# Kernel tuning notes

Hardware: AMD Instinct MI355X
Metric: run time of the kernel (lower is better)

The kernel has to match this reference:

```python
import jax, jax.numpy as jnp
import numpy as np
import math

B, S = 512, 50
L, U = 40000, 20000
D_MODEL, D_LOC, D_USR, D_T, H, D_FF = 80, 56, 12, 12, 4, 160
DH = D_MODEL // H


def _layernorm(x, g, b, eps=1e-5):
    m = x.mean(-1, keepdims=True)
    v = ((x - m) ** 2).mean(-1, keepdims=True)
    return (x - m) / jnp.sqrt(v + eps) * g + b


def setup_inputs() -> dict:
    key = jax.random.key(0)
    ks = jax.random.split(key, 16)
    loc_seq = jax.random.randint(ks[0], (B, S), 0, L)
    user_seq = jax.random.randint(ks[1], (B, S), 0, U)
    weekday_seq = jax.random.randint(ks[2], (B, S), 0, 7)
    start_min_seq = jax.random.uniform(ks[3], (B, S), jnp.float32, 0.0, 1440.0)
    dur_seq = jax.random.uniform(ks[4], (B, S), jnp.float32, 0.0, 600.0)
    diff_seq = jax.random.randint(ks[5], (B, S), 0, 7)
    mask = jnp.ones((B, S), dtype=bool)
    # sinusoidal positional-encoding buffer (60, 80), as in __init__
    pos = np.arange(60, dtype=np.float32)[:, None]
    div = np.exp(np.arange(0, D_MODEL, 2, dtype=np.float32) * (-math.log(10000.0) / D_MODEL))
    pe = np.zeros((60, D_MODEL), dtype=np.float32)
    pe[:, 0::2] = np.sin(pos * div)
    pe[:, 1::2] = np.cos(pos * div)
    g = lambda k, shape: jax.random.normal(k, shape, jnp.float32) * 0.02
    return dict(
        loc_seq=loc_seq, user_seq=user_seq, weekday_seq=weekday_seq,
        start_min_seq=start_min_seq, dur_seq=dur_seq, diff_seq=diff_seq, mask=mask,
        loc_emb=jax.random.normal(ks[6], (L, D_LOC), jnp.float32) * 0.01,
        user_emb=jax.random.normal(ks[7], (U, D_USR), jnp.float32) * 0.01,
        tproj_w=g(ks[8], (6, D_T)), tproj_b=jnp.zeros((D_T,), jnp.float32),
        in_norm_g=jnp.ones((D_MODEL,), jnp.float32), in_norm_b=jnp.zeros((D_MODEL,), jnp.float32),
        attn_in_w=g(ks[9], (3 * D_MODEL, D_MODEL)), attn_in_b=jnp.zeros((3 * D_MODEL,), jnp.float32),
        attn_out_w=g(ks[10], (D_MODEL, D_MODEL)), attn_out_b=jnp.zeros((D_MODEL,), jnp.float32),
        norm1_g=jnp.ones((D_MODEL,), jnp.float32), norm1_b=jnp.zeros((D_MODEL,), jnp.float32),
        ff_w1=g(ks[11], (D_MODEL, D_FF)), ff_b1=jnp.zeros((D_FF,), jnp.float32),
        ff_w2=g(ks[12], (D_FF, D_MODEL)), ff_b2=jnp.zeros((D_MODEL,), jnp.float32),
        norm2_g=jnp.ones((D_MODEL,), jnp.float32), norm2_b=jnp.zeros((D_MODEL,), jnp.float32),
        pred_w1=g(ks[13], (D_MODEL, D_FF)), pred_b1=jnp.zeros((D_FF,), jnp.float32),
        pred_w2=g(ks[14], (D_FF, L)), pred_b2=jnp.zeros((L,), jnp.float32),
        recency_decay=jnp.float32(0.62), freq_weight=jnp.float32(2.2),
        history_scale=jnp.float32(11.0), model_weight=jnp.float32(0.22),
        pe=jnp.asarray(pe),
    )


def _history_scores(loc_seq, mask, recency_decay, freq_weight, history_scale):
    # Vectorized scatter-max (recency) + scatter-add (frequency) over the whole
    # (B, S) index set -- replaces the per-timestep python loop of the original.
    maskf = mask.astype(jnp.float32)
    time_from_end = jnp.arange(S - 1, -1, -1, dtype=jnp.float32)  # seq_len - t - 1
    rw = jnp.power(recency_decay, time_from_end)[None, :] * maskf  # (B, S)
    bidx = jnp.broadcast_to(jnp.arange(B)[:, None], (B, S))
    rec = jnp.zeros((B, L), jnp.float32).at[bidx, loc_seq].max(rw)
    freq = jnp.zeros((B, L), jnp.float32).at[bidx, loc_seq].add(maskf)
    freq = freq / jnp.clip(freq.max(axis=1, keepdims=True), 1.0)
    return history_scale * (rec + freq_weight * freq)


def _forward(loc_seq, user_seq, weekday_seq, start_min_seq, dur_seq, diff_seq, mask,
             loc_emb, user_emb, tproj_w, tproj_b, in_norm_g, in_norm_b,
             attn_in_w, attn_in_b, attn_out_w, attn_out_b, norm1_g, norm1_b,
             ff_w1, ff_b1, ff_w2, ff_b2, norm2_g, norm2_b,
             pred_w1, pred_b1, pred_w2, pred_b2,
             recency_decay, freq_weight, history_scale, model_weight, pe):
    hist = _history_scores(loc_seq, mask, recency_decay, freq_weight, history_scale)
    le = loc_emb[loc_seq]                       # (B, S, 56)
    ue = user_emb[user_seq]                     # (B, S, 12)
    tr = (start_min_seq / 60.0) / 24.0 * 2.0 * jnp.pi
    wr = weekday_seq.astype(jnp.float32) / 7.0 * 2.0 * jnp.pi
    tf = jnp.stack([jnp.sin(tr), jnp.cos(tr), jnp.log1p(dur_seq) / 8.0,
                    jnp.sin(wr), jnp.cos(wr), diff_seq.astype(jnp.float32) / 7.0], axis=-1)
    te = tf @ tproj_w + tproj_b                 # (B, S, 12)
    x = jnp.concatenate([le, ue, te], axis=-1)  # (B, S, 80)
    x = _layernorm(x, in_norm_g, in_norm_b)
    x = x + pe[:S][None]
    # multi-head self-attention with key padding mask (dropout=eval mode)
    qkv = x @ attn_in_w.T + attn_in_b
    q, k, v = jnp.split(qkv, 3, axis=-1)
    q = q.reshape(B, S, H, DH)
    k = k.reshape(B, S, H, DH)
    v = v.reshape(B, S, H, DH)
    scores = jnp.einsum('bqhd,bkhd->bhqk', q, k) / jnp.sqrt(jnp.float32(DH))
    scores = jnp.where(mask[:, None, None, :], scores, -jnp.inf)
    attn = jax.nn.softmax(scores, axis=-1)
    ao = jnp.einsum('bhqk,bkhd->bqhd', attn, v).reshape(B, S, D_MODEL)
    ao = ao @ attn_out_w.T + attn_out_b
    x = _layernorm(x + ao, norm1_g, norm1_b)
    ff = jax.nn.gelu(x @ ff_w1 + ff_b1, approximate=False) @ ff_w2 + ff_b2
    x = _layernorm(x + ff, norm2_g, norm2_b)
    seq_lens = mask.sum(axis=1) - 1             # index of last valid token
    last = jnp.take_along_axis(x, seq_lens[:, None, None], axis=1)[:, 0]  # (B, 80)
    logits = jax.nn.gelu(last @ pred_w1 + pred_b1, approximate=False) @ pred_w2 + pred_b2
    return hist + model_weight * (jax.nn.softmax(logits, axis=1) * L)


def reference(loc_seq, user_seq, weekday_seq, start_min_seq, dur_seq, diff_seq, mask,
              loc_emb, user_emb, tproj_w, tproj_b, in_norm_g, in_norm_b,
              attn_in_w, attn_in_b, attn_out_w, attn_out_b, norm1_g, norm1_b,
              ff_w1, ff_b1, ff_w2, ff_b2, norm2_g, norm2_b,
              pred_w1, pred_b1, pred_w2, pred_b2,
              recency_decay, freq_weight, history_scale, model_weight, pe):
    return _forward(loc_seq, user_seq, weekday_seq, start_min_seq, dur_seq, diff_seq, mask,
                    loc_emb, user_emb, tproj_w, tproj_b, in_norm_g, in_norm_b,
                    attn_in_w, attn_in_b, attn_out_w, attn_out_b, norm1_g, norm1_b,
                    ff_w1, ff_b1, ff_w2, ff_b2, norm2_g, norm2_b,
                    pred_w1, pred_b1, pred_w2, pred_b2,
                    recency_decay, freq_weight, history_scale, model_weight, pe)
```

## Files before the change

### kernel.cpp

```cpp
#include <hip/hip_runtime.h>
#include <math.h>

#define BB 512
#define SS 50
#define LL 40000
#define DM 80
#define DLOC 56
#define DUSR 12
#define HH 4
#define DH 20
#define DFF 160
#define XP 81
#define NPREP 157

typedef __attribute__((ext_vector_type(8))) short short8v;
typedef __attribute__((ext_vector_type(4))) float f32x4;

__device__ __forceinline__ unsigned short f2bf(float f) {
    unsigned u = __float_as_uint(f);
    u += 0x7fffu + ((u >> 16) & 1u);
    return (unsigned short)(u >> 16);
}

__device__ __forceinline__ float gelu_exact(float x) {
    return 0.5f * x * (1.0f + erff(x * 0.70710678118654752f));
}

__global__ __launch_bounds__(256) void k_front(
        const int* __restrict__ loc_seq, const int* __restrict__ user_seq,
        const int* __restrict__ wd_seq, const float* __restrict__ start_seq,
        const float* __restrict__ dur_seq, const int* __restrict__ diff_seq,
        const float* __restrict__ loc_emb, const float* __restrict__ user_emb,
        const float* __restrict__ tproj_w, const float* __restrict__ tproj_b,
        const float* __restrict__ in_g, const float* __restrict__ in_b,
        const float* __restrict__ pe,
        const float* __restrict__ Wqkv, const float* __restrict__ bqkv,
        const float* __restrict__ aw, const float* __restrict__ ab,
        const float* __restrict__ n1g, const float* __restrict__ n1b,
        const float* __restrict__ w1, const float* __restrict__ b1,
        const float* __restrict__ w2, const float* __restrict__ b2,
        const float* __restrict__ n2g, const float* __restrict__ n2b,
        const float* __restrict__ pw1, const float* __restrict__ pb1,
        const float* __restrict__ pw2,
        const float* __restrict__ p_decay, const float* __restrict__ p_fw,
        const float* __restrict__ p_hs,
        float* __restrict__ histval, int* __restrict__ histloc,
        unsigned short* __restrict__ gvec, unsigned short* __restrict__ Bp,
        float* __restrict__ rowsum) {
    int tid = threadIdx.x;

    if (blockIdx.x >= BB) {
        int n = (blockIdx.x - BB) * 256 + tid;
        if (n < LL) {
            #pragma unroll
            for (int kq = 0; kq < 20; ++kq) {
                unsigned short pk[8];
                #pragma unroll
                for (int j = 0; j < 8; ++j)
                    pk[j] = f2bf(pw2[(size_t)(kq * 8 + j) * LL + n]);
                *(uint4*)&Bp[((size_t)kq * LL + n) * 8] = *(const uint4*)pk;
            }
        }
        return;
    }

    int b = blockIdx.x;
    int w = tid >> 6, l = tid & 63;
    __shared__ float xs[SS][XP];
    __shared__ float tf6[SS][6];
    __shared__ float rw[SS];
    __shared__ int   loc[SS];
    __shared__ int   usr[SS];
    __shared__ float qr[DM];
    __shared__ float uu[HH][DM];
    __shared__ float scw[HH][SS];
    __shared__ float wsm[HH][DM];
    __shared__ float ao[DM];
    __shared__ float v1[DM];
    __shared__ float v2[DM];
    __shared__ float f1[DFF];

    if (tid == 0) rowsum[b] = 0.f;

    if (tid < SS) {
        int t = tid;
        loc[t] = loc_seq[b * SS + t];
        usr[t] = user_seq[b * SS + t];
        float tr = start_seq[b * SS + t] * (float)(M_PI / 720.0);
        float wrd = (float)wd_seq[b * SS + t] * (float)(2.0 * M_PI / 7.0);
        tf6[t][0] = sinf(tr); tf6[t][1] = cosf(tr);
        tf6[t][2] = log1pf(dur_seq[b * SS + t]) * 0.125f;
        tf6[t][3] = sinf(wrd); tf6[t][4] = cosf(wrd);
        tf6[t][5] = (float)diff_seq[b * SS + t] * (1.f / 7.f);
        rw[t] = exp2f((float)(SS - 1 - t) * log2f(p_decay[0]));
    }
    __syncthreads();

    if (w < 3) {
        for (int idx = tid; idx < SS * DM; idx += 192) {
            int t = idx / DM, d = idx - t * DM;
            float v;
            if (d < DLOC) {
                v = loc_emb[(size_t)loc[t] * DLOC + d];
            } else if (d < DLOC + DUSR) {
                v = user_emb[(size_t)usr[t] * DUSR + (d - DLOC)];
            } else {
                int j = d - (DLOC + DUSR);
                float a = tproj_b[j];
                #pragma unroll
                for (int i = 0; i < 6; ++i) a += tf6[t][i] * tproj_w[i * 12 + j];
                v = a;
            }
            xs[t][d] = v;
        }
    } else {
        int t = l;
        int c = 0; float rmx = 0.f; int first = (t < SS) ? 1 : 0;
        if (t < SS) {
            int my = loc[t];
            for (int j = 0; j < SS; ++j) {
                if (loc[j] == my) {
                    c++; rmx = fmaxf(rmx, rw[j]);
                    if (j < t) first = 0;
                }
            }
        }
        int mc = c;
        #pragma unroll
        for (int m = 1; m < 64; m <<= 1) mc = max(mc, __shfl_xor(mc, m));
        if (t < SS) {
            float val = 0.f;
            if (first) val = p_hs[0] * (rmx + p_fw[0] * ((float)c / (float)max(mc, 1)));
            histval[b * SS + t] = val;
            histloc[b * SS + t] = loc[t];
        }
    }
    __syncthreads();

    for (int t = w; t < SS; t += 4) {
        float a0 = xs[t][l];
        float a1 = (l < 16) ? xs[t][64 + l] : 0.f;
        float sm = a0 + a1;
        #pragma unroll
        for (int m = 1; m < 64; m <<= 1) sm += __shfl_xor(sm, m);
        float mean = sm * (1.f / DM);
        float d0 = a0 - mean, d1 = (l < 16) ? (a1 - mean) : 0.f;
        float vs = d0 * d0 + d1 * d1;
        #pragma unroll
        for (int m = 1; m < 64; m <<= 1) vs += __shfl_xor(vs, m);
        float inv = rsqrtf(vs * (1.f / DM) + 1e-5f);
        xs[t][l] = d0 * inv * in_g[l] + in_b[l] + pe[t * DM + l];
        if (l < 16)
            xs[t][64 + l] = d1 * inv * in_g[64 + l] + in_b[64 + l] + pe[t * DM + 64 + l];
    }
    __syncthreads();

    {
        float xl0 = xs[49][l];
        float xl1 = (l < 16) ? xs[49][64 + l] : 0.f;
        for (int i = 0; i < 20; ++i) {
            int j = w * 20 + i;
            const float* Wr = Wqkv + (size_t)j * DM;
            float p = xl0 * Wr[l];
            if (l < 16) p += xl1 * Wr[64 + l];
            #pragma unroll
            for (int m = 1; m < 64; m <<= 1) p += __shfl_xor(p, m);
            if (l == 0) qr[j] = p + bqkv[j];
        }
    }
    __syncthreads();

    {
        int h0 = tid / DM, d0i = tid - (tid / DM) * DM;
        float a0 = 0.f;
        #pragma unroll 4
        for (int j = 0; j < DH; ++j)
            a0 += qr[h0 * DH + j] * Wqkv[(size_t)(DM + h0 * DH + j) * DM + d0i];
        uu[h0][d0i] = a0;
        if (tid < 64) {
            int idx1 = tid + 256;
            int h1 = idx1 / DM, d1i = idx1 - h1 * DM;
            float a1 = 0.f;
            #pragma unroll 4
            for (int j = 0; j < DH; ++j)
                a1 += qr[h1 * DH + j] * Wqkv[(size_t)(DM + h1 * DH + j) * DM + d1i];
            uu[h1][d1i] = a1;
        }
    }
    __syncthreads();

    if (tid < HH * SS) {
        int h = tid / SS, s = tid - (tid / SS) * SS;
        float a = 0.f;
        #pragma unroll 4
        for (int d = 0; d < DM; ++d) a += uu[h][d] * xs[s][d];
        scw[h][s] = a * 0.22360679774997896f;
    }
    __syncthreads();

    {
        float v = (l < SS) ? scw[w][l] : -1e30f;
        float m = v;
        #pragma unroll
        for (int mk = 1; mk < 64; mk <<= 1) m = fmaxf(m, __shfl_xor(m, mk));
        float e = (l < SS) ? __expf(v - m) : 0.f;
        float sm = e;
        #pragma unroll
        for (int mk = 1; mk < 64; mk <<= 1) sm += __shfl_xor(sm, mk);
        if (l < SS) scw[w][l] = e / sm;
    }
    __syncthreads();

    {
        int h0 = tid / DM, d0i = tid - (tid / DM) * DM;
        float a0 = 0.f;
        #pragma unroll 5
        for (int s = 0; s < SS; ++s) a0 += scw[h0][s] * xs[s][d0i];
        wsm[h0][d0i] = a0;
        if (tid < 64) {
            int idx1 = tid + 256;
            int h1 = idx1 / DM, d1i = idx1 - h1 * DM;
            float a1 = 0.f;
            #pragma unroll 5
            for (int s = 0; s < SS; ++s) a1 += scw[h1][s] * xs[s][d1i];
            wsm[h1][d1i] = a1;
        }
    }
    __syncthreads();

    {
        float wl0 = wsm[w][l];
        float wl1 = (l < 16) ? wsm[w][64 + l] : 0.f;
        for (int i = 0; i < 20; ++i) {
            int j = w * 20 + i;
            const float* Wr = Wqkv + (size_t)(2 * DM + j) * DM;
            float p = wl0 * Wr[l];
            if (l < 16) p += wl1 * Wr[64 + l];
            #pragma unroll
            for (int m = 1; m < 64; m <<= 1) p += __shfl_xor(p, m);
            if (l == 0) ao[j] = p + bqkv[2 * DM + j];
        }
    }
    __syncthreads();

    {
        float al0 = ao[l];
        float al1 = (l < 16) ? ao[64 + l] : 0.f;
        for (int i = 0; i < 20; ++i) {
            int j = w * 20 + i;
            const float* Wr = aw + (size_t)j * DM;
            float p = al0 * Wr[l];
            if (l < 16) p += al1 * Wr[64 + l];
            #pragma unroll
            for (int m = 1; m < 64; m <<= 1) p += __shfl_xor(p, m);
            if (l == 0) v1[j] = xs[49][j] + p + ab[j];
        }
    }
    __syncthreads();

    {
        float a0 = v1[l], a1 = (l < 16) ? v1[64 + l] : 0.f;
        float sm = a0 + a1;
        #pragma unroll
        for (int m = 1; m < 64; m <<= 1) sm += __shfl_xor(sm, m);
        float mean = sm * (1.f / DM);
        float d0 = a0 - mean, d1 = (l < 16) ? (a1 - mean) : 0.f;
        float vs = d0 * d0 + d1 * d1;
        #pragma unroll
        for (int m = 1; m < 64; m <<= 1) vs += __shfl_xor(vs, m);
        float inv = rsqrtf(vs * (1.f / DM) + 1e-5f);
        if (tid < DM) v2[tid] = (v1[tid] - mean) * inv * n1g[tid] + n1b[tid];
    }
    __syncthreads();

    if (tid < DFF) {
        float a = b1[tid];
        for (int d = 0; d < DM; ++d) a += v2[d] * w1[(size_t)d * DFF + tid];
        f1[tid] = gelu_exact(a);
    }
    __syncthreads();

    if (tid < DM) {
        float a = b2[tid];
        for (int j = 0; j < DFF; ++j) a += f1[j] * w2[(size_t)j * DM + tid];
        v1[tid] = v2[tid] + a;
    }
    __syncthreads();

    {
        float a0 = v1[l], a1 = (l < 16) ? v1[64 + l] : 0.f;
        float sm = a0 + a1;
        #pragma unroll
        for (int m = 1; m < 64; m <<= 1) sm += __shfl_xor(sm, m);
        float mean = sm * (1.f / DM);
        float d0 = a0 - mean, d1 = (l < 16) ? (a1 - mean) : 0.f;
        float vs = d0 * d0 + d1 * d1;
        #pragma unroll
        for (int m = 1; m < 64; m <<= 1) vs += __shfl_xor(vs, m);
        float inv = rsqrtf(vs * (1.f / DM) + 1e-5f);
        if (tid < DM) v2[tid] = (v1[tid] - mean) * inv * n2g[tid] + n2b[tid];
    }
    __syncthreads();

    if (tid < DFF) {
        float a = pb1[tid];
        for (int d = 0; d < DM; ++d) a += v2[d] * pw1[(size_t)d * DFF + tid];
        gvec[((size_t)(tid >> 3) * BB + b) * 8 + (tid & 7)] = f2bf(gelu_exact(a));
    }
}

template<int WRITE>
__global__ __launch_bounds__(512) void k_mfma(
        const unsigned short* __restrict__ Abf,
        const unsigned short* __restrict__ Bp,
        const float* __restrict__ bias,
        const float* __restrict__ p_mw,
        float* __restrict__ rowsum,
        float* __restrict__ out) {
    int by = blockIdx.x;
    int bx = blockIdx.y;
    int m0 = by * 256, n0 = bx * 64;
    int tid = threadIdx.x;
    int l = tid & 63, w = tid >> 6;
    int lr = l & 15, lg = l >> 4;
    int wr = (w >> 1) * 64, wc = (w & 1) * 32;
    __shared__ float prs[256][2];

    const short8v* Af = (const short8v*)Abf;
    const short8v* Bf = (const short8v*)Bp;
    f32x4 acc[4][2] = {};
    #pragma unroll
    for (int step = 0; step < 5; ++step) {
        int kq = step * 4 + lg;
        short8v b0 = Bf[(size_t)kq * LL + n0 + wc + lr];
        short8v b1 = Bf[(size_t)kq * LL + n0 + wc + 16 + lr];
        #pragma unroll
        for (int mi = 0; mi < 4; ++mi) {
            short8v a = Af[kq * BB + m0 + wr + mi * 16 + lr];
            acc[mi][0] = __builtin_amdgcn_mfma_f32_16x16x32_bf16(a, b0, acc[mi][0], 0, 0, 0);
            acc[mi][1] = __builtin_amdgcn_mfma_f32_16x16x32_bf16(a, b1, acc[mi][1], 0, 0, 0);
        }
    }
    float bia0 = bias[n0 + wc + lr];
    float bia1 = bias[n0 + wc + 16 + lr];
    if (WRITE) {
        float mwL = p_mw[0] * (float)LL;
        #pragma unroll
        for (int mi = 0; mi < 4; ++mi) {
            #pragma unroll
            for (int r = 0; r < 4; ++r) {
                int row = m0 + wr + mi * 16 + lg * 4 + r;
                float scl = mwL / rowsum[row];
                out[(size_t)row * LL + n0 + wc + lr]      = __expf(acc[mi][0][r] + bia0) * scl;
                out[(size_t)row * LL + n0 + wc + 16 + lr] = __expf(acc[mi][1][r] + bia1) * scl;
            }
        }
    } else {
        #pragma unroll
        for (int mi = 0; mi < 4; ++mi) {
            #pragma unroll
            for (int r = 0; r < 4; ++r) {
                float sv = __expf(acc[mi][0][r] + bia0) + __expf(acc[mi][1][r] + bia1);
                #pragma unroll
                for (int mk = 1; mk < 16; mk <<= 1) sv += __shfl_xor(sv, mk);
                if (lr == 0) prs[wr + mi * 16 + lg * 4 + r][w & 1] = sv;
            }
        }
        __syncthreads();
        if (tid < 256)
            atomicAdd(&rowsum[m0 + tid], prs[tid][0] + prs[tid][1]);
    }
}

__global__ void k_scatter(const float* __restrict__ histval,
                          const int* __restrict__ histloc,
                          float* __restrict__ out) {
    int b = blockIdx.x, t = threadIdx.x;
    if (t < SS) {
        float v = histval[b * SS + t];
        if (v != 0.f) atomicAdd(&out[(size_t)b * LL + histloc[b * SS + t]], v);
    }
}

extern "C" void kernel_launch(void* const* d_in, const int* in_sizes, int n_in,
                              void* d_out, int out_size, void* d_ws, size_t ws_size,
                              hipStream_t stream) {
    const int*   loc_seq   = (const int*)d_in[0];
    const int*   user_seq  = (const int*)d_in[1];
    const int*   wd_seq    = (const int*)d_in[2];
    const float* start_seq = (const float*)d_in[3];
    const float* dur_seq   = (const float*)d_in[4];
    const int*   diff_seq  = (const int*)d_in[5];
    const float* loc_emb   = (const float*)d_in[7];
    const float* user_emb  = (const float*)d_in[8];
    const float* tproj_w   = (const float*)d_in[9];
    const float* tproj_b   = (const float*)d_in[10];
    const float* in_g      = (const float*)d_in[11];
    const float* in_b      = (const float*)d_in[12];
    const float* attn_in_w = (const float*)d_in[13];
    const float* attn_in_b = (const float*)d_in[14];
    const float* attn_out_w= (const float*)d_in[15];
    const float* attn_out_b= (const float*)d_in[16];
    const float* n1g       = (const float*)d_in[17];
    const float* n1b       = (const float*)d_in[18];
    const float* ff_w1     = (const float*)d_in[19];
    const float* ff_b1     = (const float*)d_in[20];
    const float* ff_w2     = (const float*)d_in[21];
    const float* ff_b2     = (const float*)d_in[22];
    const float* n2g       = (const float*)d_in[23];
    const float* n2b       = (const float*)d_in[24];
    const float* pw1       = (const float*)d_in[25];
    const float* pb1       = (const float*)d_in[26];
    const float* pw2       = (const float*)d_in[27];
    const float* pb2       = (const float*)d_in[28];
    const float* p_decay   = (const float*)d_in[29];
    const float* p_fw      = (const float*)d_in[30];
    const float* p_hs      = (const float*)d_in[31];
    const float* p_mw      = (const float*)d_in[32];
    const float* pe        = (const float*)d_in[33];
    float* out = (float*)d_out;

    char* base = (char*)d_ws;
    unsigned short* Bp = (unsigned short*)base;
    float* rowsum  = (float*)(base + (size_t)LL * DFF * 2);
    float* histval = rowsum + 512;
    int*   histloc = (int*)(histval + 25600);
    unsigned short* gvec = (unsigned short*)(histloc + 25600);

    k_front<<<BB + NPREP, 256, 0, stream>>>(loc_seq, user_seq, wd_seq, start_seq,
                                            dur_seq, diff_seq, loc_emb, user_emb,
                                            tproj_w, tproj_b, in_g, in_b, pe,
                                            attn_in_w, attn_in_b, attn_out_w, attn_out_b,
                                            n1g, n1b, ff_w1, ff_b1, ff_w2, ff_b2,
                                            n2g, n2b, pw1, pb1, pw2,
                                            p_decay, p_fw, p_hs,
                                            histval, histloc, gvec, Bp, rowsum);
    dim3 g4(2, 625);
    k_mfma<0><<<g4, 512, 0, stream>>>(gvec, Bp, pb2, p_mw, rowsum, out);
    k_mfma<1><<<g4, 512, 0, stream>>>(gvec, Bp, pb2, p_mw, rowsum, out);
    k_scatter<<<BB, 64, 0, stream>>>(histval, histloc, out);
}
```

Before: 303.2 us.

## Stage attention weights in LDS and tile MFMA GEMM through shared memory

In the front kernel, the Q, V and output-projection weight matrices are now loaded coalesced into a padded shared-memory tile, with the next load overlapped with earlier compute. One thread per output row then computes each matvec, replacing per-row wave shuffle reductions. The MFMA logits kernel moves to 128-row tiles with 256 threads, staging A and B operands through LDS before the MFMA loop instead of reading them directly from global memory. This is meant to cut redundant global reads and shuffle overhead, at the cost of more LDS use, register staging, and twice as many GEMM blocks.

```diff
diff --git a/kernel.cpp b/kernel.cpp
--- a/kernel.cpp
+++ b/kernel.cpp
@@ -26,7 +26,7 @@
     return 0.5f * x * (1.0f + erff(x * 0.70710678118654752f));
 }
 
-__global__ __launch_bounds__(256) void k_front(
+__global__ __launch_bounds__(256, 2) void k_front(
         const int* __restrict__ loc_seq, const int* __restrict__ user_seq,
         const int* __restrict__ wd_seq, const float* __restrict__ start_seq,
         const float* __restrict__ dur_seq, const int* __restrict__ diff_seq,
@@ -67,6 +67,7 @@
     int b = blockIdx.x;
     int w = tid >> 6, l = tid & 63;
     __shared__ float xs[SS][XP];
+    __shared__ float WA[DM * XP];
     __shared__ float tf6[SS][6];
     __shared__ float rw[SS];
     __shared__ int   loc[SS];
@@ -137,6 +138,9 @@
     }
     __syncthreads();
 
+    float stg[25];
+    #pragma unroll
+    for (int i = 0; i < 25; ++i) stg[i] = Wqkv[i * 256 + tid];
     for (int t = w; t < SS; t += 4) {
         float a0 = xs[t][l];
         float a1 = (l < 16) ? xs[t][64 + l] : 0.f;
@@ -153,23 +157,24 @@
         if (l < 16)
             xs[t][64 + l] = d1 * inv * in_g[64 + l] + in_b[64 + l] + pe[t * DM + 64 + l];
     }
-    __syncthreads();
-
-    {
-        float xl0 = xs[49][l];
-        float xl1 = (l < 16) ? xs[49][64 + l] : 0.f;
-        for (int i = 0; i < 20; ++i) {
-            int j = w * 20 + i;
-            const float* Wr = Wqkv + (size_t)j * DM;
-            float p = xl0 * Wr[l];
-            if (l < 16) p += xl1 * Wr[64 + l];
-            #pragma unroll
-            for (int m = 1; m < 64; m <<= 1) p += __shfl_xor(p, m);
-            if (l == 0) qr[j] = p + bqkv[j];
-        }
-    }
-    __syncthreads();
-
+    #pragma unroll
+    for (int i = 0; i < 25; ++i) {
+        int g = i * 256 + tid;
+        WA[(g / DM) * XP + (g - (g / DM) * DM)] = stg[i];
+    }
+    __syncthreads();
+
+    if (tid < DM) {
+        float a = bqkv[tid];
+        const float* Wl = &WA[tid * XP];
+        #pragma unroll 8
+        for (int d = 0; d < DM; ++d) a += xs[49][d] * Wl[d];
+        qr[tid] = a;
+    }
+    __syncthreads();
+
+    #pragma unroll
+    for (int i = 0; i < 25; ++i) stg[i] = Wqkv[2 * DM * DM + i * 256 + tid];
     {
         int h0 = tid / DM, d0i = tid - (tid / DM) * DM;
         float a0 = 0.f;
@@ -187,6 +192,11 @@
             uu[h1][d1i] = a1;
         }
     }
+    #pragma unroll
+    for (int i = 0; i < 25; ++i) {
+        int g = i * 256 + tid;
+        WA[(g / DM) * XP + (g - (g / DM) * DM)] = stg[i];
+    }
     __syncthreads();
 
     if (tid < HH * SS) {
@@ -228,33 +238,31 @@
     }
     __syncthreads();
 
-    {
-        float wl0 = wsm[w][l];
-        float wl1 = (l < 16) ? wsm[w][64 + l] : 0.f;
-        for (int i = 0; i < 20; ++i) {
-            int j = w * 20 + i;
-            const float* Wr = Wqkv + (size_t)(2 * DM + j) * DM;
-            float p = wl0 * Wr[l];
-            if (l < 16) p += wl1 * Wr[64 + l];
-            #pragma unroll
-            for (int m = 1; m < 64; m <<= 1) p += __shfl_xor(p, m);
-            if (l == 0) ao[j] = p + bqkv[2 * DM + j];
-        }
-    }
-    __syncthreads();
-
-    {
-        float al0 = ao[l];
-        float al1 = (l < 16) ? ao[64 + l] : 0.f;
-        for (int i = 0; i < 20; ++i) {
-            int j = w * 20 + i;
-            const float* Wr = aw + (size_t)j * DM;
-            float p = al0 * Wr[l];
-            if (l < 16) p += al1 * Wr[64 + l];
-            #pragma unroll
-            for (int m = 1; m < 64; m <<= 1) p += __shfl_xor(p, m);
-            if (l == 0) v1[j] = xs[49][j] + p + ab[j];
-        }
+    if (tid < DM) {
+        int h = tid / DH;
+        float a = bqkv[2 * DM + tid];
+        const float* Wl = &WA[tid * XP];
+        #pragma unroll 8
+        for (int d = 0; d < DM; ++d) a += Wl[d] * wsm[h][d];
+        ao[tid] = a;
+    }
+    __syncthreads();
+
+    #pragma unroll
+    for (int i = 0; i < 25; ++i) stg[i] = aw[i * 256 + tid];
+    #pragma unroll
+    for (int i = 0; i < 25; ++i) {
+        int g = i * 256 + tid;
+        WA[(g / DM) * XP + (g - (g / DM) * DM)] = stg[i];
+    }
+    __syncthreads();
+
+    if (tid < DM) {
+        float a = ab[tid];
+        const float* Wl = &WA[tid * XP];
+        #pragma unroll 8
+        for (int d = 0; d < DM; ++d) a += ao[d] * Wl[d];
+        v1[tid] = xs[49][tid] + a;
     }
     __syncthreads();
 
@@ -310,7 +318,7 @@
 }
 
 template<int WRITE>
-__global__ __launch_bounds__(512) void k_mfma(
+__global__ __launch_bounds__(256, 2) void k_mfma(
         const unsigned short* __restrict__ Abf,
         const unsigned short* __restrict__ Bp,
         const float* __restrict__ bias,
@@ -319,24 +327,43 @@
         float* __restrict__ out) {
     int by = blockIdx.x;
     int bx = blockIdx.y;
-    int m0 = by * 256, n0 = bx * 64;
+    int m0 = by * 128, n0 = bx * 64;
     int tid = threadIdx.x;
     int l = tid & 63, w = tid >> 6;
     int lr = l & 15, lg = l >> 4;
     int wr = (w >> 1) * 64, wc = (w & 1) * 32;
-    __shared__ float prs[256][2];
-
-    const short8v* Af = (const short8v*)Abf;
-    const short8v* Bf = (const short8v*)Bp;
+    __shared__ uint4 As4[2560];
+    __shared__ uint4 Bs4[1280];
+    __shared__ float prs[128][2];
+
+    uint4 ra[10], rb[5];
+    #pragma unroll
+    for (int i = 0; i < 10; ++i) {
+        int g = i * 256 + tid; int kq = g >> 7, row = g & 127;
+        ra[i] = *(const uint4*)&Abf[((size_t)kq * BB + m0 + row) * 8];
+    }
+    #pragma unroll
+    for (int i = 0; i < 5; ++i) {
+        int g = i * 256 + tid; int kq = g >> 6, col = g & 63;
+        rb[i] = *(const uint4*)&Bp[((size_t)kq * LL + n0 + col) * 8];
+    }
+    #pragma unroll
+    for (int i = 0; i < 10; ++i) As4[i * 256 + tid] = ra[i];
+    #pragma unroll
+    for (int i = 0; i < 5; ++i) Bs4[i * 256 + tid] = rb[i];
+    __syncthreads();
+
+    const short8v* Asv = (const short8v*)As4;
+    const short8v* Bsv = (const short8v*)Bs4;
     f32x4 acc[4][2] = {};
     #pragma unroll
-    for (int step = 0; step < 5; ++step) {
-        int kq = step * 4 + lg;
-        short8v b0 = Bf[(size_t)kq * LL + n0 + wc + lr];
-        short8v b1 = Bf[(size_t)kq * LL + n0 + wc + 16 + lr];
+    for (int st = 0; st < 5; ++st) {
+        int kq = st * 4 + lg;
+        short8v b0 = Bsv[kq * 64 + wc + lr];
+        short8v b1 = Bsv[kq * 64 + wc + 16 + lr];
         #pragma unroll
         for (int mi = 0; mi < 4; ++mi) {
-            short8v a = Af[kq * BB + m0 + wr + mi * 16 + lr];
+            short8v a = Asv[kq * 128 + wr + mi * 16 + lr];
             acc[mi][0] = __builtin_amdgcn_mfma_f32_16x16x32_bf16(a, b0, acc[mi][0], 0, 0, 0);
             acc[mi][1] = __builtin_amdgcn_mfma_f32_16x16x32_bf16(a, b1, acc[mi][1], 0, 0, 0);
         }
@@ -367,7 +394,7 @@
             }
         }
         __syncthreads();
-        if (tid < 256)
+        if (tid < 128)
             atomicAdd(&rowsum[m0 + tid], prs[tid][0] + prs[tid][1]);
     }
 }
@@ -435,8 +462,8 @@
                                             n2g, n2b, pw1, pb1, pw2,
                                             p_decay, p_fw, p_hs,
                                             histval, histloc, gvec, Bp, rowsum);
-    dim3 g4(2, 625);
-    k_mfma<0><<<g4, 512, 0, stream>>>(gvec, Bp, pb2, p_mw, rowsum, out);
-    k_mfma<1><<<g4, 512, 0, stream>>>(gvec, Bp, pb2, p_mw, rowsum, out);
+    dim3 g4(4, 625);
+    k_mfma<0><<<g4, 256, 0, stream>>>(gvec, Bp, pb2, p_mw, rowsum, out);
+    k_mfma<1><<<g4, 256, 0, stream>>>(gvec, Bp, pb2, p_mw, rowsum, out);
     k_scatter<<<BB, 64, 0, stream>>>(histval, histloc, out);
 }
```

Result: faster. 267.5 us (-11.8%).
